# Kernel optimization log

Measured on AMD Instinct MI355X. Metric: run time of the kernel, lower is better.

The kernel has to match this reference:

```python
import jax, jax.numpy as jnp
import numpy as np

B, S, D, H = 2, 2048, 1024, 16
DK = D // H


def setup_inputs() -> dict:
    key = jax.random.key(0)
    ks = jax.random.split(key, 12)
    q = jax.random.normal(ks[0], (B, S, D), dtype=jnp.float32)
    k = jax.random.normal(ks[1], (B, S, D), dtype=jnp.float32)
    v = jax.random.normal(ks[2], (B, S, D), dtype=jnp.float32)
    # causal mask: 1 = attend, 0 = masked (masked_fill(mask==0, -inf))
    mask = jnp.tril(jnp.ones((S, S), dtype=jnp.int32))[None, None]
    w = 0.02
    Wq = jax.random.normal(ks[3], (D, D), dtype=jnp.float32) * w
    bq = jnp.zeros((D,), dtype=jnp.float32)
    Wk = jax.random.normal(ks[4], (D, D), dtype=jnp.float32) * w
    bk = jnp.zeros((D,), dtype=jnp.float32)
    Wv = jax.random.normal(ks[5], (D, D), dtype=jnp.float32) * w
    bv = jnp.zeros((D,), dtype=jnp.float32)
    Wo = jax.random.normal(ks[6], (D, D), dtype=jnp.float32) * w
    bo = jnp.zeros((D,), dtype=jnp.float32)
    return {"q": q, "k": k, "v": v, "mask": mask,
            "Wq": Wq, "bq": bq, "Wk": Wk, "bk": bk,
            "Wv": Wv, "bv": bv, "Wo": Wo, "bo": bo}


def _split_heads(x):
    b, s, _ = x.shape
    return x.reshape(b, s, H, DK).transpose(0, 2, 1, 3)  # [B,H,S,DK]


def reference(q, k, v, mask, Wq, bq, Wk, bk, Wv, bv, Wo, bo):
    qh = _split_heads(q @ Wq.T + bq)
    kh = _split_heads(k @ Wk.T + bk)
    vh = _split_heads(v @ Wv.T + bv)
    scale = 1.0 / jnp.sqrt(jnp.float32(DK))
    scores = jnp.einsum("bhqd,bhkd->bhqk", qh, kh) * scale  # [B,H,S,S]
    scores = jnp.where(mask == 0, -jnp.inf, scores)
    pesos = jax.nn.softmax(scores, axis=-1)
    pesos = jnp.nan_to_num(pesos, nan=0.0)  # fully-masked rows -> 0
    out = jnp.einsum("bhqk,bhkd->bhqd", pesos, vh)
    out = out.transpose(0, 2, 1, 3).reshape(q.shape[0], q.shape[1], D)
    # dropout is identity at inference
    return out @ Wo.T + bo
```

## Files before the change

### kernel.cpp

```cpp
#include <hip/hip_runtime.h>
#include <hip/hip_bf16.h>

#define B_  2
#define S_  2048
#define D_  1024
#define H_  16
#define DK_ 64

using bf16 = __hip_bfloat16;
typedef __bf16 bf16x8 __attribute__((ext_vector_type(8)));
typedef float  f32x4  __attribute__((ext_vector_type(4)));

__device__ inline void st1(float* p, float v) { *p = v; }
__device__ inline void st1(bf16*  p, float v) { *p = __float2bfloat16(v); }

__device__ inline void gll16(const bf16* g, bf16* l) {
    __builtin_amdgcn_global_load_lds(
        (const __attribute__((address_space(1))) unsigned int*)g,
        (__attribute__((address_space(3))) unsigned int*)l, 16, 0, 0);
}

__global__ __launch_bounds__(256) void cvt_kernel(
    const float* __restrict__ s0, const float* __restrict__ s1,
    const float* __restrict__ s2, const float* __restrict__ s3,
    const float* __restrict__ s4, const float* __restrict__ s5,
    const float* __restrict__ s6,
    bf16* __restrict__ d0, bf16* __restrict__ d1, bf16* __restrict__ d2,
    bf16* __restrict__ d3, bf16* __restrict__ d4, bf16* __restrict__ d5,
    bf16* __restrict__ d6, int nbig, int nsmall)
{
    const int z = blockIdx.y;
    const float* s; bf16* d; int n;
    switch (z) {
        case 0: s = s0; d = d0; n = nbig;   break;
        case 1: s = s1; d = d1; n = nbig;   break;
        case 2: s = s2; d = d2; n = nbig;   break;
        case 3: s = s3; d = d3; n = nsmall; break;
        case 4: s = s4; d = d4; n = nsmall; break;
        case 5: s = s5; d = d5; n = nsmall; break;
        default: s = s6; d = d6; n = nsmall; break;
    }
    const int idx = (blockIdx.x * 256 + threadIdx.x) * 4;
    if (idx < n) {
        const float4 v = *reinterpret_cast<const float4*>(s + idx);
        union { ushort4 u; __bf16 h[4]; } r;
        r.h[0] = (__bf16)v.x; r.h[1] = (__bf16)v.y;
        r.h[2] = (__bf16)v.z; r.h[3] = (__bf16)v.w;
        *reinterpret_cast<ushort4*>(d + idx) = r.u;
    }
}

template <typename TC, bool VT3>
__global__ __launch_bounds__(256, 3) void gemm_bt_kernel(
    const bf16* __restrict__ A0, const bf16* __restrict__ A1, const bf16* __restrict__ A2,
    const bf16* __restrict__ W0, const bf16* __restrict__ W1, const bf16* __restrict__ W2,
    const float* __restrict__ b0, const float* __restrict__ b1, const float* __restrict__ b2,
    TC* __restrict__ C0, TC* __restrict__ C1, TC* __restrict__ C2,
    int M, int N, int K)
{
    const int z = blockIdx.z;
    const bf16*  A    = (z == 0) ? A0 : (z == 1) ? A1 : A2;
    const bf16*  W    = (z == 0) ? W0 : (z == 1) ? W1 : W2;
    const float* bias = (z == 0) ? b0 : (z == 1) ? b1 : b2;
    TC*          C    = (z == 0) ? C0 : (z == 1) ? C1 : C2;

    __shared__ bf16 As[128][32];
    __shared__ bf16 Bs[128][32];

    const int t    = threadIdx.x;
    const int lane = t & 63;
    const int wave = t >> 6;
    const int quad = lane >> 4;
    const int l16  = lane & 15;
    const int wm   = wave >> 1;
    const int wn   = wave & 1;

    const int m0 = blockIdx.y * 128;
    const int n0 = blockIdx.x * 128;

    const int r0 = wave * 32 + (lane >> 2);
    const int c0 = (lane & 3) * 8;
    const bf16* Ab = A + (size_t)(m0 + r0) * K + c0;
    const bf16* Bb = W + (size_t)(n0 + r0) * K + c0;
    bf16* asd = &As[wave * 32][0];
    bf16* bsd = &Bs[wave * 32][0];

    f32x4 acc[4][4] = {};

    for (int kt = 0; kt < K; kt += 32) {
        __syncthreads();
        gll16(Ab + kt,           asd);
        gll16(Ab + 16 * K + kt,  asd + 16 * 32);
        gll16(Bb + kt,           bsd);
        gll16(Bb + 16 * K + kt,  bsd + 16 * 32);
        __syncthreads();

        bf16x8 af[4], bfr[4];
#pragma unroll
        for (int mi = 0; mi < 4; mi++)
            af[mi] = *reinterpret_cast<const bf16x8*>(&As[wm * 64 + mi * 16 + l16][quad * 8]);
#pragma unroll
        for (int ni = 0; ni < 4; ni++)
            bfr[ni] = *reinterpret_cast<const bf16x8*>(&Bs[wn * 64 + ni * 16 + l16][quad * 8]);
#pragma unroll
        for (int mi = 0; mi < 4; mi++)
#pragma unroll
            for (int ni = 0; ni < 4; ni++)
                acc[mi][ni] = __builtin_amdgcn_mfma_f32_16x16x32_bf16(
                    af[mi], bfr[ni], acc[mi][ni], 0, 0, 0);
    }

    if (VT3 && z == 2) {
#pragma unroll
        for (int ni = 0; ni < 4; ni++) {
            const int col = n0 + wn * 64 + ni * 16 + l16;
            const float bvv = bias[col];
            const int hh = col >> 6, dh = col & 63;
#pragma unroll
            for (int mi = 0; mi < 4; mi++) {
                const int rb  = m0 + wm * 64 + mi * 16 + quad * 4;
                const int bb  = rb >> 11;
                const int tok = rb & (S_ - 1);
                union { ushort4 u; __bf16 h[4]; } pk;
#pragma unroll
                for (int i = 0; i < 4; i++)
                    pk.h[i] = (__bf16)(acc[mi][ni][i] + bvv);
                bf16* vt = (bf16*)C + ((size_t)(bb * H_ + hh) * DK_ + dh) * S_ + tok;
                *reinterpret_cast<ushort4*>(vt) = pk.u;
            }
        }
    } else {
#pragma unroll
        for (int ni = 0; ni < 4; ni++) {
            const int col = n0 + wn * 64 + ni * 16 + l16;
            const float bvv = bias[col];
#pragma unroll
            for (int mi = 0; mi < 4; mi++) {
#pragma unroll
                for (int i = 0; i < 4; i++) {
                    const int row = m0 + wm * 64 + mi * 16 + quad * 4 + i;
                    st1(&C[(size_t)row * N + col], acc[mi][ni][i] + bvv);
                }
            }
        }
    }
}

__global__ __launch_bounds__(256, 3) void attn_kernel(
    const bf16* __restrict__ Qp, const bf16* __restrict__ Kp,
    const bf16* __restrict__ VT, bf16* __restrict__ AO)
{
    const int t    = threadIdx.x;
    const int lane = t & 63;
    const int wave = t >> 6;
    const int quad = lane >> 4;
    const int l16  = lane & 15;

    const int pairi  = blockIdx.x;
    const int tLong  = 31 - pairi;
    const int tShort = pairi;
    const int h = blockIdx.y;
    const int b = blockIdx.z;
    const size_t bh = (size_t)b * S_ * D_ + (size_t)h * DK_;
    const bf16* vtb = VT + (size_t)(b * H_ + h) * DK_ * S_;

    __shared__ bf16 Ks[2][64][64];
    __shared__ bf16 Vs[2][64][64];
    __shared__ bf16 Pb[4][16][72];

    const int sR = lane >> 3;
    const int scg = ((lane & 7) ^ sR) * 8;
    const int swz0 = (quad ^ (l16 & 7)) * 8;
    const int swz1 = ((quad + 4) ^ (l16 & 7)) * 8;

    const float QSC = 0.18033688f;
    const float NEG = -1e30f;

    bf16x8 onesf;
#pragma unroll
    for (int j = 0; j < 8; j++) onesf[j] = (__bf16)1.0f;

    int til = tLong;
    bf16x8 qf0, qf1;
    {
        const bf16* qrow = Qp + bh + (size_t)(til * 64 + wave * 16 + l16) * D_;
        qf0 = *reinterpret_cast<const bf16x8*>(qrow + quad * 8);
        qf1 = *reinterpret_cast<const bf16x8*>(qrow + 32 + quad * 8);
#pragma unroll
        for (int j = 0; j < 8; j++) {
            qf0[j] = (__bf16)((float)qf0[j] * QSC);
            qf1[j] = (__bf16)((float)qf1[j] * QSC);
        }
    }

    f32x4 lacc = {};
    f32x4 oacc[4] = {};

    const int nA   = tLong + 1;
    const int ntot = 33;

    {
#pragma unroll
        for (int j = 0; j < 2; j++) {
            const int R = wave * 16 + j * 8 + sR;
            gll16(Kp + bh + (size_t)R * D_ + scg, &Ks[0][wave * 16 + j * 8][0]);
            gll16(vtb + (size_t)R * S_ + scg,     &Vs[0][wave * 16 + j * 8][0]);
        }
    }

    int kcbase = 0;
    for (int it = 0; it < ntot; it++) {
        __syncthreads();

        if (it + 1 < ntot) {
            const int itn = it + 1;
            const int k0n = ((itn < nA) ? itn : itn - nA) * 64;
            const int bufn = itn & 1;
#pragma unroll
            for (int j = 0; j < 2; j++) {
                const int R = wave * 16 + j * 8 + sR;
                gll16(Kp + bh + (size_t)(k0n + R) * D_ + scg, &Ks[bufn][wave * 16 + j * 8][0]);
                gll16(vtb + (size_t)R * S_ + k0n + scg,       &Vs[bufn][wave * 16 + j * 8][0]);
            }
        }

        if (it == nA) {
            const int qw0 = til * 64 + wave * 16;
#pragma unroll
            for (int i = 0; i < 4; i++) {
                const float inv = 1.0f / lacc[i];
#pragma unroll
                for (int n = 0; n < 4; n++)
                    AO[bh + (size_t)(qw0 + quad * 4 + i) * D_ + n * 16 + l16] =
                        __float2bfloat16(oacc[n][i] * inv);
            }
            til = tShort; kcbase = nA;
            const bf16* qrow = Qp + bh + (size_t)(til * 64 + wave * 16 + l16) * D_;
            qf0 = *reinterpret_cast<const bf16x8*>(qrow + quad * 8);
            qf1 = *reinterpret_cast<const bf16x8*>(qrow + 32 + quad * 8);
#pragma unroll
            for (int j = 0; j < 8; j++) {
                qf0[j] = (__bf16)((float)qf0[j] * QSC);
                qf1[j] = (__bf16)((float)qf1[j] * QSC);
            }
            lacc = f32x4{};
#pragma unroll
            for (int n = 0; n < 4; n++) oacc[n] = f32x4{};
        }

        const int kc  = it - kcbase;
        const int k0  = kc * 64;
        const int buf = it & 1;
        const int qw0 = til * 64 + wave * 16;

        f32x4 sc[4];
#pragma unroll
        for (int ch = 0; ch < 4; ch++) {
            const int row = ch * 16 + l16;
            bf16x8 kfa = *reinterpret_cast<const bf16x8*>(&Ks[buf][row][swz0]);
            bf16x8 kfb = *reinterpret_cast<const bf16x8*>(&Ks[buf][row][swz1]);
            f32x4 zz = {};
            zz = __builtin_amdgcn_mfma_f32_16x16x32_bf16(qf0, kfa, zz, 0, 0, 0);
            sc[ch] = __builtin_amdgcn_mfma_f32_16x16x32_bf16(qf1, kfb, zz, 0, 0, 0);
        }

        const bool bnd = (kc == til);
#pragma unroll
        for (int i = 0; i < 4; i++) {
            const int r = quad * 4 + i;
            float s0 = sc[0][i], s1 = sc[1][i], s2 = sc[2][i], s3 = sc[3][i];
            if (bnd) {
                const int qi = qw0 + r;
                s0 = (k0 + l16      <= qi) ? s0 : NEG;
                s1 = (k0 + 16 + l16 <= qi) ? s1 : NEG;
                s2 = (k0 + 32 + l16 <= qi) ? s2 : NEG;
                s3 = (k0 + 48 + l16 <= qi) ? s3 : NEG;
            }
            Pb[wave][r][l16]      = __float2bfloat16(__builtin_amdgcn_exp2f(s0));
            Pb[wave][r][16 + l16] = __float2bfloat16(__builtin_amdgcn_exp2f(s1));
            Pb[wave][r][32 + l16] = __float2bfloat16(__builtin_amdgcn_exp2f(s2));
            Pb[wave][r][48 + l16] = __float2bfloat16(__builtin_amdgcn_exp2f(s3));
        }
        asm volatile("s_waitcnt lgkmcnt(0)" ::: "memory");
        bf16x8 pf0 = *reinterpret_cast<const bf16x8*>(&Pb[wave][l16][quad * 8]);
        bf16x8 pf1 = *reinterpret_cast<const bf16x8*>(&Pb[wave][l16][32 + quad * 8]);

        lacc = __builtin_amdgcn_mfma_f32_16x16x32_bf16(pf0, onesf, lacc, 0, 0, 0);
        lacc = __builtin_amdgcn_mfma_f32_16x16x32_bf16(pf1, onesf, lacc, 0, 0, 0);

#pragma unroll
        for (int n = 0; n < 4; n++) {
            const int row = n * 16 + l16;
            bf16x8 vt0 = *reinterpret_cast<const bf16x8*>(&Vs[buf][row][swz0]);
            bf16x8 vt1 = *reinterpret_cast<const bf16x8*>(&Vs[buf][row][swz1]);
            oacc[n] = __builtin_amdgcn_mfma_f32_16x16x32_bf16(pf0, vt0, oacc[n], 0, 0, 0);
            oacc[n] = __builtin_amdgcn_mfma_f32_16x16x32_bf16(pf1, vt1, oacc[n], 0, 0, 0);
        }
    }

    {
        const int qw0 = til * 64 + wave * 16;
#pragma unroll
        for (int i = 0; i < 4; i++) {
            const float inv = 1.0f / lacc[i];
#pragma unroll
            for (int n = 0; n < 4; n++)
                AO[bh + (size_t)(qw0 + quad * 4 + i) * D_ + n * 16 + l16] =
                    __float2bfloat16(oacc[n][i] * inv);
        }
    }
}

extern "C" void kernel_launch(void* const* d_in, const int* in_sizes, int n_in,
                              void* d_out, int out_size, void* d_ws, size_t ws_size,
                              hipStream_t stream)
{
    const float* q  = (const float*)d_in[0];
    const float* k  = (const float*)d_in[1];
    const float* v  = (const float*)d_in[2];
    const float* Wq = (const float*)d_in[4];
    const float* bq = (const float*)d_in[5];
    const float* Wk = (const float*)d_in[6];
    const float* bk = (const float*)d_in[7];
    const float* Wv = (const float*)d_in[8];
    const float* bv = (const float*)d_in[9];
    const float* Wo = (const float*)d_in[10];
    const float* bo = (const float*)d_in[11];
    float* out = (float*)d_out;

    bf16* ws = (bf16*)d_ws;
    const size_t MD = (size_t)(B_ * S_) * D_;
    const size_t WN = (size_t)D_ * D_;
    bf16* qb  = ws;
    bf16* kb  = ws + MD;
    bf16* vb  = ws + 2 * MD;
    bf16* wqb = ws + 3 * MD;
    bf16* wkb = wqb + WN;
    bf16* wvb = wkb + WN;
    bf16* wob = wvb + WN;
    bf16* Qp  = wob + WN;
    bf16* Kp  = Qp + MD;
    bf16* VT  = Kp + MD;
    bf16* AO  = Qp;

    const int M = B_ * S_;

    cvt_kernel<<<dim3((int)(MD / 4 / 256), 7), 256, 0, stream>>>(
        q, k, v, Wq, Wk, Wv, Wo, qb, kb, vb, wqb, wkb, wvb, wob,
        (int)MD, (int)WN);

    gemm_bt_kernel<bf16, true><<<dim3(D_ / 128, M / 128, 3), 256, 0, stream>>>(
        qb, kb, vb, wqb, wkb, wvb, bq, bk, bv, Qp, Kp, VT, M, D_, D_);

    attn_kernel<<<dim3(16, H_, B_), 256, 0, stream>>>(Qp, Kp, VT, AO);

    gemm_bt_kernel<float, false><<<dim3(D_ / 128, M / 128, 1), 256, 0, stream>>>(
        AO, AO, AO, wob, wob, wob, bo, bo, bo, out, out, out, M, D_, D_);
}
```

Measured before the change: 237.9 us.

## Unpair causal attention tiles and use 64-row tiles for output projection

The attention kernel stops pairing a long and a short causal query tile per block and launches one block per query tile (32 per head), each looping over only its needed key tiles. The output-projection GEMM gets a BM template parameter and runs with 64-row tiles, doubling its grid so more blocks fill the GPU. In exchange, attention blocks now have unequal amounts of work, and the smaller GEMM tile reuses each loaded weight tile across fewer rows.

Result: slower. 258.3 us (+8.6%).

```diff
diff --git a/kernel.cpp b/kernel.cpp
--- a/kernel.cpp
+++ b/kernel.cpp
@@ -50,8 +50,8 @@
     }
 }
 
-template <typename TC, bool VT3>
-__global__ __launch_bounds__(256, 3) void gemm_bt_kernel(
+template <typename TC, bool VT3, int BM>
+__global__ __launch_bounds__(256, BM == 128 ? 3 : 4) void gemm_bt_kernel(
     const bf16* __restrict__ A0, const bf16* __restrict__ A1, const bf16* __restrict__ A2,
     const bf16* __restrict__ W0, const bf16* __restrict__ W1, const bf16* __restrict__ W2,
     const float* __restrict__ b0, const float* __restrict__ b1, const float* __restrict__ b2,
@@ -64,7 +64,7 @@
     const float* bias = (z == 0) ? b0 : (z == 1) ? b1 : b2;
     TC*          C    = (z == 0) ? C0 : (z == 1) ? C1 : C2;
 
-    __shared__ bf16 As[128][32];
+    __shared__ bf16 As[BM][32];
     __shared__ bf16 Bs[128][32];
 
     const int t    = threadIdx.x;
@@ -75,35 +75,38 @@
     const int wm   = wave >> 1;
     const int wn   = wave & 1;
 
-    const int m0 = blockIdx.y * 128;
+    const int m0 = blockIdx.y * BM;
     const int n0 = blockIdx.x * 128;
 
-    const int r0 = wave * 32 + (lane >> 2);
-    const int c0 = (lane & 3) * 8;
-    const bf16* Ab = A + (size_t)(m0 + r0) * K + c0;
-    const bf16* Bb = W + (size_t)(n0 + r0) * K + c0;
-    bf16* asd = &As[wave * 32][0];
+    constexpr int RPW = BM / 4;
+    constexpr int MI  = BM / 32;
+    const int ar0 = wave * RPW + (lane >> 2);
+    const int br0 = wave * 32  + (lane >> 2);
+    const int c0  = (lane & 3) * 8;
+    const bf16* Ab = A + (size_t)(m0 + ar0) * K + c0;
+    const bf16* Bb = W + (size_t)(n0 + br0) * K + c0;
+    bf16* asd = &As[wave * RPW][0];
     bf16* bsd = &Bs[wave * 32][0];
 
-    f32x4 acc[4][4] = {};
+    f32x4 acc[MI][4] = {};
 
     for (int kt = 0; kt < K; kt += 32) {
         __syncthreads();
-        gll16(Ab + kt,           asd);
-        gll16(Ab + 16 * K + kt,  asd + 16 * 32);
-        gll16(Bb + kt,           bsd);
-        gll16(Bb + 16 * K + kt,  bsd + 16 * 32);
+        gll16(Ab + kt, asd);
+        if constexpr (BM == 128) gll16(Ab + 16 * K + kt, asd + 16 * 32);
+        gll16(Bb + kt, bsd);
+        gll16(Bb + 16 * K + kt, bsd + 16 * 32);
         __syncthreads();
 
-        bf16x8 af[4], bfr[4];
-#pragma unroll
-        for (int mi = 0; mi < 4; mi++)
-            af[mi] = *reinterpret_cast<const bf16x8*>(&As[wm * 64 + mi * 16 + l16][quad * 8]);
+        bf16x8 af[MI], bfr[4];
+#pragma unroll
+        for (int mi = 0; mi < MI; mi++)
+            af[mi] = *reinterpret_cast<const bf16x8*>(&As[wm * (BM / 2) + mi * 16 + l16][quad * 8]);
 #pragma unroll
         for (int ni = 0; ni < 4; ni++)
             bfr[ni] = *reinterpret_cast<const bf16x8*>(&Bs[wn * 64 + ni * 16 + l16][quad * 8]);
 #pragma unroll
-        for (int mi = 0; mi < 4; mi++)
+        for (int mi = 0; mi < MI; mi++)
 #pragma unroll
             for (int ni = 0; ni < 4; ni++)
                 acc[mi][ni] = __builtin_amdgcn_mfma_f32_16x16x32_bf16(
@@ -117,8 +120,8 @@
             const float bvv = bias[col];
             const int hh = col >> 6, dh = col & 63;
 #pragma unroll
-            for (int mi = 0; mi < 4; mi++) {
-                const int rb  = m0 + wm * 64 + mi * 16 + quad * 4;
+            for (int mi = 0; mi < MI; mi++) {
+                const int rb  = m0 + wm * (BM / 2) + mi * 16 + quad * 4;
                 const int bb  = rb >> 11;
                 const int tok = rb & (S_ - 1);
                 union { ushort4 u; __bf16 h[4]; } pk;
@@ -135,10 +138,10 @@
             const int col = n0 + wn * 64 + ni * 16 + l16;
             const float bvv = bias[col];
 #pragma unroll
-            for (int mi = 0; mi < 4; mi++) {
+            for (int mi = 0; mi < MI; mi++) {
 #pragma unroll
                 for (int i = 0; i < 4; i++) {
-                    const int row = m0 + wm * 64 + mi * 16 + quad * 4 + i;
+                    const int row = m0 + wm * (BM / 2) + mi * 16 + quad * 4 + i;
                     st1(&C[(size_t)row * N + col], acc[mi][ni][i] + bvv);
                 }
             }
@@ -156,9 +159,7 @@
     const int quad = lane >> 4;
     const int l16  = lane & 15;
 
-    const int pairi  = blockIdx.x;
-    const int tLong  = 31 - pairi;
-    const int tShort = pairi;
+    const int til = 31 - blockIdx.x;
     const int h = blockIdx.y;
     const int b = blockIdx.z;
     const size_t bh = (size_t)b * S_ * D_ + (size_t)h * DK_;
@@ -180,7 +181,6 @@
 #pragma unroll
     for (int j = 0; j < 8; j++) onesf[j] = (__bf16)1.0f;
 
-    int til = tLong;
     bf16x8 qf0, qf1;
     {
         const bf16* qrow = Qp + bh + (size_t)(til * 64 + wave * 16 + l16) * D_;
@@ -196,8 +196,7 @@
     f32x4 lacc = {};
     f32x4 oacc[4] = {};
 
-    const int nA   = tLong + 1;
-    const int ntot = 33;
+    const int ntot = til + 1;
 
     {
 #pragma unroll
@@ -208,14 +207,12 @@
         }
     }
 
-    int kcbase = 0;
     for (int it = 0; it < ntot; it++) {
         __syncthreads();
 
         if (it + 1 < ntot) {
-            const int itn = it + 1;
-            const int k0n = ((itn < nA) ? itn : itn - nA) * 64;
-            const int bufn = itn & 1;
+            const int k0n = (it + 1) * 64;
+            const int bufn = (it + 1) & 1;
 #pragma unroll
             for (int j = 0; j < 2; j++) {
                 const int R = wave * 16 + j * 8 + sR;
@@ -224,32 +221,7 @@
             }
         }
 
-        if (it == nA) {
-            const int qw0 = til * 64 + wave * 16;
-#pragma unroll
-            for (int i = 0; i < 4; i++) {
-                const float inv = 1.0f / lacc[i];
-#pragma unroll
-                for (int n = 0; n < 4; n++)
-                    AO[bh + (size_t)(qw0 + quad * 4 + i) * D_ + n * 16 + l16] =
-                        __float2bfloat16(oacc[n][i] * inv);
-            }
-            til = tShort; kcbase = nA;
-            const bf16* qrow = Qp + bh + (size_t)(til * 64 + wave * 16 + l16) * D_;
-            qf0 = *reinterpret_cast<const bf16x8*>(qrow + quad * 8);
-            qf1 = *reinterpret_cast<const bf16x8*>(qrow + 32 + quad * 8);
-#pragma unroll
-            for (int j = 0; j < 8; j++) {
-                qf0[j] = (__bf16)((float)qf0[j] * QSC);
-                qf1[j] = (__bf16)((float)qf1[j] * QSC);
-            }
-            lacc = f32x4{};
-#pragma unroll
-            for (int n = 0; n < 4; n++) oacc[n] = f32x4{};
-        }
-
-        const int kc  = it - kcbase;
-        const int k0  = kc * 64;
+        const int k0  = it * 64;
         const int buf = it & 1;
         const int qw0 = til * 64 + wave * 16;
 
@@ -264,7 +236,7 @@
             sc[ch] = __builtin_amdgcn_mfma_f32_16x16x32_bf16(qf1, kfb, zz, 0, 0, 0);
         }
 
-        const bool bnd = (kc == til);
+        const bool bnd = (it == til);
 #pragma unroll
         for (int i = 0; i < 4; i++) {
             const int r = quad * 4 + i;
@@ -349,11 +321,11 @@
         q, k, v, Wq, Wk, Wv, Wo, qb, kb, vb, wqb, wkb, wvb, wob,
         (int)MD, (int)WN);
 
-    gemm_bt_kernel<bf16, true><<<dim3(D_ / 128, M / 128, 3), 256, 0, stream>>>(
+    gemm_bt_kernel<bf16, true, 128><<<dim3(D_ / 128, M / 128, 3), 256, 0, stream>>>(
         qb, kb, vb, wqb, wkb, wvb, bq, bk, bv, Qp, Kp, VT, M, D_, D_);
 
-    attn_kernel<<<dim3(16, H_, B_), 256, 0, stream>>>(Qp, Kp, VT, AO);
-
-    gemm_bt_kernel<float, false><<<dim3(D_ / 128, M / 128, 1), 256, 0, stream>>>(
+    attn_kernel<<<dim3(32, H_, B_), 256, 0, stream>>>(Qp, Kp, VT, AO);
+
+    gemm_bt_kernel<float, false, 64><<<dim3(D_ / 128, M / 64, 1), 256, 0, stream>>>(
         AO, AO, AO, wob, wob, wob, bo, bo, bo, out, out, out, M, D_, D_);
 }
```
